# Kernel optimization log

Hardware: AMD Instinct MI355X
Metric: run time of the kernel (lower is better)

The kernel has to match this reference:

```python
import jax, jax.numpy as jnp
import numpy as np

B, K, D = 16384, 64, 128


def setup_inputs() -> dict:
    key = jax.random.key(0)
    kx, kc = jax.random.split(key)
    x = jax.random.normal(kx, (B, D), dtype=jnp.float32)
    centers = jax.random.uniform(kc, (K, D), dtype=jnp.float32)  # torch.rand init
    return {"x": x, "centers": centers}


def reference(x, centers):
    batch, dim = x.shape
    k = centers.shape[0]
    # pairwise squared distances, same math as sum((x - c)^2)
    diff = x[:, None, :] - centers[None, :, :]          # [B, K, D]
    dist_sq = jnp.sum(diff * diff, axis=-1)             # [B, K]
    expo = -0.5 * dist_sq
    # safe softmax over clusters (identical to max-subtracted exp/sum)
    resp = jax.nn.softmax(expo, axis=-1)                # [B, K]
    log_resp = jnp.log(jnp.clip(resp, 1e-8))
    # hard assignment and per-cluster statistics
    assign = jnp.argmin(dist_sq, axis=-1)               # [B] int
    onehot = jax.nn.one_hot(assign, k, dtype=x.dtype)   # [B, K]
    cluster_weight = jnp.sum(onehot, axis=0)            # [K]
    emp_total = jnp.einsum('nk,nd->kd', onehot, x)      # [K, D]
    emp_mean = emp_total / (cluster_weight[:, None] + 1e-7)
    # masked centered samples: onehot[n,k]*(x_n - mean_k) is nonzero only at k=assign(n)
    xm = x - emp_mean[assign]                           # [B, D]
    covar_total = jnp.einsum('nk,nd,ne->kde', onehot, xm, xm)  # [K, D, D]
    covar = covar_total / (cluster_weight[:, None, None] + 1e-7)
    eye = jnp.eye(dim, dtype=x.dtype)
    covar_diag = covar * eye
    covar_off = covar * (1.0 - eye)
    diag_dist_sq = jnp.sum((covar_diag - eye) ** 2, axis=(1, 2))  # [K]
    off_dist_sq = jnp.sum(covar_off ** 2, axis=(1, 2))            # [K]
    mean_dist_sq = jnp.sum((emp_mean - centers) ** 2, axis=1)     # [K]
    mean_mse = jnp.sum(cluster_weight * mean_dist_sq) / (batch * dim)
    covar_mse = jnp.sum(
        cluster_weight * diag_dist_sq / (batch * dim)
        + cluster_weight * off_dist_sq / (batch * dim * (dim - 1.0))
    )
    return log_resp, mean_mse, covar_mse
```

## Files before the change

kernel.cpp:

```cpp
#include <hip/hip_runtime.h>

#define BB 16384
#define KK 64
#define DD 128
#define SEG 256
#define MAXITEMS 128
#define NRB 4
#define RSLAB 4096
#define RBLKS (KK * NRB)

typedef __attribute__((ext_vector_type(8))) short bf16x8;
typedef __attribute__((ext_vector_type(4))) float f32x4;

__device__ __forceinline__ unsigned int packbf2(float a, float b) {
    unsigned ua = __float_as_uint(a);
    unsigned ub = __float_as_uint(b);
    ua = (ua + 0x7FFFu + ((ua >> 16) & 1u)) >> 16;
    ub = (ub + 0x7FFFu + ((ub >> 16) & 1u)) >> 16;
    return ua | (ub << 16);
}

__global__ __launch_bounds__(256) void k_rows(
    const float* __restrict__ x, const float* __restrict__ centers,
    float* __restrict__ log_resp, int* __restrict__ assign,
    int* __restrict__ bhist, int* __restrict__ counter)
{
    __shared__ float xs[64][132];
    __shared__ float ct[DD][66];
    __shared__ float cn2[KK];
    __shared__ int   lh[KK];

    const int tid = threadIdx.x;
    const int row0 = blockIdx.x * 64;

    if (blockIdx.x == 0 && tid == 0) *counter = 0;
    if (tid < KK) lh[tid] = 0;

    for (int g = tid; g < 64 * 32; g += 256) {
        int r = g >> 5, c4 = g & 31;
        float4 v = ((const float4*)(x + (size_t)(row0 + r) * DD))[c4];
        *(float4*)&xs[r][c4 * 4] = v;
    }
    for (int g = tid; g < KK * 32; g += 256) {
        int k = g >> 5, c4 = g & 31;
        float4 v = ((const float4*)(centers + (size_t)k * DD))[c4];
        ct[c4 * 4 + 0][k] = v.x;
        ct[c4 * 4 + 1][k] = v.y;
        ct[c4 * 4 + 2][k] = v.z;
        ct[c4 * 4 + 3][k] = v.w;
    }
    __syncthreads();
    if (tid < KK) {
        float s = 0.f;
        for (int d = 0; d < DD; ++d) { float c = ct[d][tid]; s = fmaf(c, c, s); }
        cn2[tid] = s;
    }
    __syncthreads();

    const int tr = tid >> 5;
    const int tc = tid & 31;
    const int k0 = tc * 2, k1 = k0 + 1;

    float acc0[8], acc1[8];
    #pragma unroll
    for (int i = 0; i < 8; ++i) { acc0[i] = 0.f; acc1[i] = 0.f; }

    for (int d = 0; d < DD; d += 4) {
        float2 b0 = *(const float2*)&ct[d + 0][k0];
        float2 b1 = *(const float2*)&ct[d + 1][k0];
        float2 b2 = *(const float2*)&ct[d + 2][k0];
        float2 b3 = *(const float2*)&ct[d + 3][k0];
        #pragma unroll
        for (int i = 0; i < 8; ++i) {
            float4 a = *(const float4*)&xs[tr * 8 + i][d];
            acc0[i] = fmaf(a.x, b0.x, acc0[i]);
            acc1[i] = fmaf(a.x, b0.y, acc1[i]);
            acc0[i] = fmaf(a.y, b1.x, acc0[i]);
            acc1[i] = fmaf(a.y, b1.y, acc1[i]);
            acc0[i] = fmaf(a.z, b2.x, acc0[i]);
            acc1[i] = fmaf(a.z, b2.y, acc1[i]);
            acc0[i] = fmaf(a.w, b3.x, acc0[i]);
            acc1[i] = fmaf(a.w, b3.y, acc1[i]);
        }
    }

    const float cn0 = 0.5f * cn2[k0], cn1 = 0.5f * cn2[k1];
    #pragma unroll
    for (int i = 0; i < 8; ++i) {
        int row = row0 + tr * 8 + i;
        float v0 = acc0[i] - cn0;
        float v1 = acc1[i] - cn1;
        float m; int idx;
        if (v1 > v0) { m = v1; idx = k1; } else { m = v0; idx = k0; }
        #pragma unroll
        for (int off = 1; off < 32; off <<= 1) {
            float ov = __shfl_xor(m, off);
            int   oi = __shfl_xor(idx, off);
            if (ov > m || (ov == m && oi < idx)) { m = ov; idx = oi; }
        }
        float s = expf(v0 - m) + expf(v1 - m);
        #pragma unroll
        for (int off = 1; off < 32; off <<= 1) s += __shfl_xor(s, off);
        float ls = logf(s);
        float lr0 = fmaxf(v0 - m - ls, -18.4206807f);
        float lr1 = fmaxf(v1 - m - ls, -18.4206807f);
        *(float2*)&log_resp[(size_t)row * KK + k0] = make_float2(lr0, lr1);
        if (tc == 0) {
            assign[row] = idx;
            atomicAdd(&lh[idx], 1);
        }
    }
    __syncthreads();
    if (tid < KK) bhist[blockIdx.x * KK + tid] = lh[tid];
}

__global__ __launch_bounds__(256) void k_scat(
    const int* __restrict__ assign, const int* __restrict__ bhist,
    int* __restrict__ sorted, float* __restrict__ cw,
    int4* __restrict__ items, int* __restrict__ item_count,
    int* __restrict__ ist, int* __restrict__ ien)
{
    __shared__ int ph_tot[4][KK], ph_pre[4][KK];
    __shared__ int cnt_s[KK], pre_s[KK], base_s[KK], cur_s[KK];

    const int tid = threadIdx.x;
    const int b = blockIdx.x;
    const int t = tid & 63, q = tid >> 6;

    int tot = 0, pre = 0;
    const int bb0 = q * 64;
    for (int bb = bb0; bb < bb0 + 64; ++bb) {
        int v = bhist[bb * KK + t];
        tot += v;
        if (bb < b) pre += v;
    }
    ph_tot[q][t] = tot; ph_pre[q][t] = pre;
    __syncthreads();

    if (tid < KK) {
        cnt_s[tid] = ph_tot[0][tid] + ph_tot[1][tid] + ph_tot[2][tid] + ph_tot[3][tid];
        pre_s[tid] = ph_pre[0][tid] + ph_pre[1][tid] + ph_pre[2][tid] + ph_pre[3][tid];
        cur_s[tid] = 0;
    }
    __syncthreads();
    if (tid == 0) {
        int base = 0;
        for (int k = 0; k < KK; ++k) { base_s[k] = base; base += cnt_s[k]; }
    }
    __syncthreads();

    if (tid < 64) {
        int r = b * 64 + tid;
        int a = assign[r];
        int p = base_s[a] + pre_s[a] + atomicAdd(&cur_s[a], 1);
        sorted[p] = r;
    }

    if (b == 0) {
        if (tid < KK) cw[tid] = (float)cnt_s[tid];
        if (tid == 0) {
            int ic = 0;
            for (int k = 0; k < KK; ++k) {
                ist[k] = ic;
                int c = cnt_s[k];
                for (int s = 0; s < c; s += SEG) {
                    int4 it; it.x = k; it.y = base_s[k] + s;
                    it.z = min(SEG, c - s); it.w = 0;
                    items[ic++] = it;
                }
                ien[k] = ic;
            }
            *item_count = ic;
        }
    }
}

__global__ __launch_bounds__(256) void k_seg(
    const float* __restrict__ x, const int* __restrict__ sorted,
    const int4* __restrict__ items, const int* __restrict__ item_count,
    float* __restrict__ part, float* __restrict__ emp_part)
{
    if ((int)blockIdx.x >= *item_count) return;
    int4 it = items[blockIdx.x];
    const int gstart = it.y, len = it.z;

    __shared__ int rows_s[128];
    __shared__ unsigned int XT[DD][68];

    const int tid = threadIdx.x;
    const int w = tid >> 6, lane = tid & 63;
    const int c4 = lane & 15, q = lane >> 4;

    f32x4 acc[2][8];
    #pragma unroll
    for (int h = 0; h < 2; ++h)
        #pragma unroll
        for (int nt = 0; nt < 8; ++nt)
            acc[h][nt] = (f32x4){0.f, 0.f, 0.f, 0.f};
    float colsum = 0.f;

    for (int half = 0; half < 2; ++half) {
        const int hoff = half * 128;
        const int hlen = min(128, len - hoff);
        if (hlen <= 0) break;

        __syncthreads();
        if (tid < hlen) rows_s[tid] = sorted[gstart + hoff + tid];
        __syncthreads();

        {
            const int r0 = 2 * lane, r1 = 2 * lane + 1;
            const int d0 = w * 32;
            const float* p0 = x + (size_t)rows_s[r0 < hlen ? r0 : 0] * DD + d0;
            const float* p1 = x + (size_t)rows_s[r1 < hlen ? r1 : 0] * DD + d0;
            #pragma unroll
            for (int i = 0; i < 8; ++i) {
                float4 a = make_float4(0.f, 0.f, 0.f, 0.f);
                float4 b = make_float4(0.f, 0.f, 0.f, 0.f);
                if (r0 < hlen) a = *(const float4*)(p0 + 4 * i);
                if (r1 < hlen) b = *(const float4*)(p1 + 4 * i);
                XT[d0 + 4 * i + 0][lane] = packbf2(a.x, b.x);
                XT[d0 + 4 * i + 1][lane] = packbf2(a.y, b.y);
                XT[d0 + 4 * i + 2][lane] = packbf2(a.z, b.z);
                XT[d0 + 4 * i + 3][lane] = packbf2(a.w, b.w);
            }
        }
        __syncthreads();

        if (tid < DD) {
            float s = 0.f;
            #pragma unroll
            for (int j4 = 0; j4 < 16; ++j4) {
                uint4 v = *(const uint4*)&XT[tid][j4 * 4];
                s += __uint_as_float(v.x << 16) + __uint_as_float(v.x & 0xFFFF0000u);
                s += __uint_as_float(v.y << 16) + __uint_as_float(v.y & 0xFFFF0000u);
                s += __uint_as_float(v.z << 16) + __uint_as_float(v.z & 0xFFFF0000u);
                s += __uint_as_float(v.w << 16) + __uint_as_float(v.w & 0xFFFF0000u);
            }
            colsum += s;
        }

        #pragma unroll
        for (int c = 0; c < 4; ++c) {
            const int ku = c * 16 + q * 4;
            bf16x8 a0 = *(const bf16x8*)&XT[(2 * w + 0) * 16 + c4][ku];
            bf16x8 a1 = *(const bf16x8*)&XT[(2 * w + 1) * 16 + c4][ku];
            #pragma unroll
            for (int nt = 0; nt < 8; ++nt) {
                bf16x8 b = *(const bf16x8*)&XT[nt * 16 + c4][ku];
                acc[0][nt] = __builtin_amdgcn_mfma_f32_16x16x32_bf16(a0, b, acc[0][nt], 0, 0, 0);
                acc[1][nt] = __builtin_amdgcn_mfma_f32_16x16x32_bf16(a1, b, acc[1][nt], 0, 0, 0);
            }
        }
    }

    if (tid < DD) emp_part[blockIdx.x * DD + tid] = colsum;

    float* pb = part + (size_t)blockIdx.x * (DD * DD);
    #pragma unroll
    for (int h = 0; h < 2; ++h) {
        const int m0 = (2 * w + h) * 16 + q * 4;
        #pragma unroll
        for (int nt = 0; nt < 8; ++nt) {
            const int n = nt * 16 + c4;
            pb[(m0 + 0) * DD + n] = acc[h][nt].x;
            pb[(m0 + 1) * DD + n] = acc[h][nt].y;
            pb[(m0 + 2) * DD + n] = acc[h][nt].z;
            pb[(m0 + 3) * DD + n] = acc[h][nt].w;
        }
    }
}

__global__ __launch_bounds__(256) void k_redfinal(
    const float* __restrict__ part, const float* __restrict__ emp_part,
    const float* __restrict__ cw, const float* __restrict__ centers,
    const int* __restrict__ ist, const int* __restrict__ ien,
    float2* __restrict__ spart, int* __restrict__ counter,
    float* __restrict__ outscalars)
{
    const int k = blockIdx.x >> 2;
    const int p = blockIdx.x & 3;
    const int i0 = ist[k], i1 = ien[k];
    const int tid = threadIdx.x;
    const int w = tid >> 6, lane = tid & 63;
    const float wgt = cw[k];
    const float inv = 1.0f / (wgt + 1e-7f);

    __shared__ float mu_s[DD], emp_s[DD];
    __shared__ float emp2[2][DD];
    __shared__ float red[4][RSLAB];

    {
        const int dh = tid & 127, hf = tid >> 7;
        float e0 = 0.f, e1 = 0.f;
        int it = i0 + hf;
        for (; it + 2 < i1; it += 4) {
            e0 += emp_part[it * DD + dh];
            e1 += emp_part[(it + 2) * DD + dh];
        }
        if (it < i1) e0 += emp_part[it * DD + dh];
        emp2[hf][dh] = e0 + e1;
    }
    __syncthreads();
    if (tid < DD) {
        float e = emp2[0][tid] + emp2[1][tid];
        emp_s[tid] = e;
        mu_s[tid] = e * inv;
    }

    float4 acc[16];
    #pragma unroll
    for (int c = 0; c < 16; ++c) acc[c] = make_float4(0.f, 0.f, 0.f, 0.f);

    const int base = p * RSLAB;
    for (int it = i0 + w; it < i1; it += 4) {
        const float* pb = part + (size_t)it * (DD * DD) + base;
        #pragma unroll
        for (int c = 0; c < 16; ++c) {
            float4 v = *(const float4*)&pb[c * 256 + lane * 4];
            acc[c].x += v.x; acc[c].y += v.y; acc[c].z += v.z; acc[c].w += v.w;
        }
    }
    #pragma unroll
    for (int c = 0; c < 16; ++c)
        *(float4*)&red[w][c * 256 + lane * 4] = acc[c];
    __syncthreads();

    float ds = 0.f, os = 0.f, mm = 0.f;
    #pragma unroll
    for (int jj = 0; jj < 16; ++jj) {
        int el = jj * 256 + tid;
        float sx = red[0][el] + red[1][el] + red[2][el] + red[3][el];
        int gel = base + el;
        int d = gel >> 7, e = gel & 127;
        float ctv = sx - mu_s[d] * emp_s[e] - emp_s[d] * mu_s[e]
                  + wgt * mu_s[d] * mu_s[e];
        float v = ctv * inv;
        if (d == e) { float t = v - 1.f; ds += t * t; }
        else        { os += v * v; }
    }
    if (p == 0 && tid < DD) {
        float t = mu_s[tid] - centers[k * DD + tid];
        mm = t * t;
    }

    #pragma unroll
    for (int off = 32; off > 0; off >>= 1) {
        ds += __shfl_down(ds, off);
        os += __shfl_down(os, off);
        mm += __shfl_down(mm, off);
    }
    __shared__ float rds[4], ros[4], rmm[4];
    __shared__ int is_last;
    if (lane == 0) { rds[w] = ds; ros[w] = os; rmm[w] = mm; }
    __syncthreads();
    if (tid == 0) {
        float DS = rds[0] + rds[1] + rds[2] + rds[3];
        float OS = ros[0] + ros[1] + ros[2] + ros[3];
        float MM = rmm[0] + rmm[1] + rmm[2] + rmm[3];
        const float bd = (float)BB * (float)DD;
        float2 mine;
        mine.x = wgt * MM / bd;
        mine.y = wgt * DS / bd + wgt * OS / (bd * (float)(DD - 1));
        spart[blockIdx.x] = mine;
        __threadfence();
        int old = atomicAdd(counter, 1);
        is_last = (old == RBLKS - 1);
    }
    __syncthreads();
    if (is_last) {
        __threadfence();
        float2 v = (tid < RBLKS) ? spart[tid] : make_float2(0.f, 0.f);
        float a = v.x, b = v.y;
        #pragma unroll
        for (int off = 32; off > 0; off >>= 1) {
            a += __shfl_down(a, off);
            b += __shfl_down(b, off);
        }
        __shared__ float ra[4], rb[4];
        if (lane == 0) { ra[w] = a; rb[w] = b; }
        __syncthreads();
        if (tid == 0) {
            outscalars[0] = ra[0] + ra[1] + ra[2] + ra[3];
            outscalars[1] = rb[0] + rb[1] + rb[2] + rb[3];
        }
    }
}

extern "C" void kernel_launch(void* const* d_in, const int* in_sizes, int n_in,
                              void* d_out, int out_size, void* d_ws, size_t ws_size,
                              hipStream_t stream) {
    const float* x = (const float*)d_in[0];
    const float* centers = (const float*)d_in[1];
    float* out = (float*)d_out;
    float* outscalars = out + (size_t)BB * KK;

    char* ws = (char*)d_ws;
    size_t off = 0;
    float*  part     = (float*)(ws + off); off += (size_t)MAXITEMS * DD * DD * 4;
    float*  emp_part = (float*)(ws + off); off += MAXITEMS * DD * 4;
    int*    sorted   = (int*)  (ws + off); off += BB * 4;
    int*    assign   = (int*)  (ws + off); off += BB * 4;
    int*    bhist    = (int*)  (ws + off); off += 256 * KK * 4;
    int4*   items    = (int4*) (ws + off); off += 256 * 16;
    float*  cw       = (float*)(ws + off); off += 256;
    int*    itemcnt  = (int*)  (ws + off); off += 256;
    int*    ist      = (int*)  (ws + off); off += 256;
    int*    ien      = (int*)  (ws + off); off += 256;
    float2* spart    = (float2*)(ws + off); off += RBLKS * 8;
    int*    counter  = (int*)  (ws + off); off += 256;

    k_rows    <<<256, 256, 0, stream>>>(x, centers, out, assign, bhist, counter);
    k_scat    <<<256, 256, 0, stream>>>(assign, bhist, sorted, cw, items,
                                        itemcnt, ist, ien);
    k_seg     <<<MAXITEMS, 256, 0, stream>>>(x, sorted, items, itemcnt,
                                             part, emp_part);
    k_redfinal<<<RBLKS, 256, 0, stream>>>(part, emp_part, cw, centers, ist, ien,
                                          spart, counter, outscalars);
}
```

Measured before the change: 126.5 us.

## Fuse scatter, segment GEMM and reduction into one kernel with grid barrier

Merges the three post-assignment kernels into one persistent 256-block kernel. Each block recomputes the cluster histogram and segment table itself and gathers its segment's row indices by ballot-scanning the assign array, so the global sorted array is no longer needed. A software grid barrier on an atomic counter then separates the covariance-GEMM phase from the reduction phase. This removes two launches and the sorted/items round trips. In exchange every block scans up to all of assign, and the spin barrier assumes all 256 blocks are co-resident.

```diff
diff --git a/kernel.cpp b/kernel.cpp
--- a/kernel.cpp
+++ b/kernel.cpp
@@ -7,7 +7,7 @@
 #define MAXITEMS 128
 #define NRB 4
 #define RSLAB 4096
-#define RBLKS (KK * NRB)
+#define NBLK 256
 
 typedef __attribute__((ext_vector_type(8))) short bf16x8;
 typedef __attribute__((ext_vector_type(4))) float f32x4;
@@ -23,7 +23,7 @@
 __global__ __launch_bounds__(256) void k_rows(
     const float* __restrict__ x, const float* __restrict__ centers,
     float* __restrict__ log_resp, int* __restrict__ assign,
-    int* __restrict__ bhist, int* __restrict__ counter)
+    int* __restrict__ bhist, int* __restrict__ counters)
 {
     __shared__ float xs[64][132];
     __shared__ float ct[DD][66];
@@ -33,7 +33,7 @@
     const int tid = threadIdx.x;
     const int row0 = blockIdx.x * 64;
 
-    if (blockIdx.x == 0 && tid == 0) *counter = 0;
+    if (blockIdx.x == 0 && tid < 2) counters[tid] = 0;
     if (tid < KK) lh[tid] = 0;
 
     for (int g = tid; g < 64 * 32; g += 256) {
@@ -114,275 +114,276 @@
     if (tid < KK) bhist[blockIdx.x * KK + tid] = lh[tid];
 }
 
-__global__ __launch_bounds__(256) void k_scat(
-    const int* __restrict__ assign, const int* __restrict__ bhist,
-    int* __restrict__ sorted, float* __restrict__ cw,
-    int4* __restrict__ items, int* __restrict__ item_count,
-    int* __restrict__ ist, int* __restrict__ ien)
+__global__ __launch_bounds__(256) void k_main(
+    const float* __restrict__ x, const int* __restrict__ assign,
+    const int* __restrict__ bhist, const float* __restrict__ centers,
+    float* __restrict__ part, float* __restrict__ emp_part,
+    float2* __restrict__ spart, int* __restrict__ counters,
+    float* __restrict__ outscalars)
 {
-    __shared__ int ph_tot[4][KK], ph_pre[4][KK];
-    __shared__ int cnt_s[KK], pre_s[KK], base_s[KK], cur_s[KK];
+    __shared__ __align__(16) char smem[65536];
+    unsigned int (*XT)[68] = (unsigned int (*)[68])smem;
+    int* rows_s = (int*)(smem + 34816);
+    float (*red)[RSLAB] = (float (*)[RSLAB])smem;
+
+    __shared__ int ph_tot[4][KK];
+    __shared__ int cnt_s[KK], ist_s[KK], ien_s[KK];
+    __shared__ int wtot[4];
+    __shared__ int myk_s, myseg_s;
 
     const int tid = threadIdx.x;
     const int b = blockIdx.x;
-    const int t = tid & 63, q = tid >> 6;
-
-    int tot = 0, pre = 0;
-    const int bb0 = q * 64;
-    for (int bb = bb0; bb < bb0 + 64; ++bb) {
-        int v = bhist[bb * KK + t];
-        tot += v;
-        if (bb < b) pre += v;
-    }
-    ph_tot[q][t] = tot; ph_pre[q][t] = pre;
-    __syncthreads();
-
-    if (tid < KK) {
+    const int w = tid >> 6, lane = tid & 63;
+    int* bar1 = counters;
+    int* fincnt = counters + 1;
+
+    {
+        const int t = tid & 63, q = tid >> 6;
+        int tot = 0;
+        for (int bb = q * 64; bb < q * 64 + 64; ++bb)
+            tot += bhist[bb * KK + t];
+        ph_tot[q][t] = tot;
+    }
+    __syncthreads();
+    if (tid < KK)
         cnt_s[tid] = ph_tot[0][tid] + ph_tot[1][tid] + ph_tot[2][tid] + ph_tot[3][tid];
-        pre_s[tid] = ph_pre[0][tid] + ph_pre[1][tid] + ph_pre[2][tid] + ph_pre[3][tid];
-        cur_s[tid] = 0;
-    }
     __syncthreads();
     if (tid == 0) {
-        int base = 0;
-        for (int k = 0; k < KK; ++k) { base_s[k] = base; base += cnt_s[k]; }
-    }
-    __syncthreads();
-
-    if (tid < 64) {
-        int r = b * 64 + tid;
-        int a = assign[r];
-        int p = base_s[a] + pre_s[a] + atomicAdd(&cur_s[a], 1);
-        sorted[p] = r;
-    }
-
-    if (b == 0) {
-        if (tid < KK) cw[tid] = (float)cnt_s[tid];
-        if (tid == 0) {
-            int ic = 0;
-            for (int k = 0; k < KK; ++k) {
-                ist[k] = ic;
-                int c = cnt_s[k];
-                for (int s = 0; s < c; s += SEG) {
-                    int4 it; it.x = k; it.y = base_s[k] + s;
-                    it.z = min(SEG, c - s); it.w = 0;
-                    items[ic++] = it;
+        int ic = 0;
+        myk_s = -1;
+        for (int k = 0; k < KK; ++k) {
+            ist_s[k] = ic;
+            int ns = (cnt_s[k] + SEG - 1) / SEG;
+            if (b >= ic && b < ic + ns) { myk_s = k; myseg_s = b - ic; }
+            ic += ns;
+            ien_s[k] = ic;
+        }
+    }
+    __syncthreads();
+
+    if (myk_s >= 0) {
+        const int kC = myk_s;
+        const int lo = myseg_s * SEG;
+        const int hi = min(lo + SEG, cnt_s[kC]);
+        const int len = hi - lo;
+
+        {
+            int running = 0;
+            for (int c = 0; c < BB / 256; ++c) {
+                if (running >= hi) break;
+                int a = assign[c * 256 + tid];
+                bool m = (a == kC);
+                unsigned long long bal = __ballot(m);
+                if (lane == 0) wtot[w] = __popcll(bal);
+                __syncthreads();
+                int woff = 0;
+                #pragma unroll
+                for (int j = 0; j < 4; ++j) if (j < w) woff += wtot[j];
+                int ctot = wtot[0] + wtot[1] + wtot[2] + wtot[3];
+                if (m) {
+                    int rank = __popcll(bal & ((1ull << lane) - 1ull));
+                    int pos = running + woff + rank;
+                    if (pos >= lo && pos < hi) rows_s[pos - lo] = c * 256 + tid;
                 }
-                ien[k] = ic;
-            }
-            *item_count = ic;
-        }
-    }
-}
-
-__global__ __launch_bounds__(256) void k_seg(
-    const float* __restrict__ x, const int* __restrict__ sorted,
-    const int4* __restrict__ items, const int* __restrict__ item_count,
-    float* __restrict__ part, float* __restrict__ emp_part)
-{
-    if ((int)blockIdx.x >= *item_count) return;
-    int4 it = items[blockIdx.x];
-    const int gstart = it.y, len = it.z;
-
-    __shared__ int rows_s[128];
-    __shared__ unsigned int XT[DD][68];
-
-    const int tid = threadIdx.x;
-    const int w = tid >> 6, lane = tid & 63;
-    const int c4 = lane & 15, q = lane >> 4;
-
-    f32x4 acc[2][8];
-    #pragma unroll
-    for (int h = 0; h < 2; ++h)
-        #pragma unroll
-        for (int nt = 0; nt < 8; ++nt)
-            acc[h][nt] = (f32x4){0.f, 0.f, 0.f, 0.f};
-    float colsum = 0.f;
-
-    for (int half = 0; half < 2; ++half) {
-        const int hoff = half * 128;
-        const int hlen = min(128, len - hoff);
-        if (hlen <= 0) break;
-
-        __syncthreads();
-        if (tid < hlen) rows_s[tid] = sorted[gstart + hoff + tid];
-        __syncthreads();
-
-        {
-            const int r0 = 2 * lane, r1 = 2 * lane + 1;
-            const int d0 = w * 32;
-            const float* p0 = x + (size_t)rows_s[r0 < hlen ? r0 : 0] * DD + d0;
-            const float* p1 = x + (size_t)rows_s[r1 < hlen ? r1 : 0] * DD + d0;
+                running += ctot;
+                __syncthreads();
+            }
+        }
+
+        const int c4 = lane & 15, q = lane >> 4;
+        f32x4 acc[2][8];
+        #pragma unroll
+        for (int h = 0; h < 2; ++h)
             #pragma unroll
-            for (int i = 0; i < 8; ++i) {
-                float4 a = make_float4(0.f, 0.f, 0.f, 0.f);
-                float4 b = make_float4(0.f, 0.f, 0.f, 0.f);
-                if (r0 < hlen) a = *(const float4*)(p0 + 4 * i);
-                if (r1 < hlen) b = *(const float4*)(p1 + 4 * i);
-                XT[d0 + 4 * i + 0][lane] = packbf2(a.x, b.x);
-                XT[d0 + 4 * i + 1][lane] = packbf2(a.y, b.y);
-                XT[d0 + 4 * i + 2][lane] = packbf2(a.z, b.z);
-                XT[d0 + 4 * i + 3][lane] = packbf2(a.w, b.w);
-            }
-        }
-        __syncthreads();
-
-        if (tid < DD) {
-            float s = 0.f;
+            for (int nt = 0; nt < 8; ++nt)
+                acc[h][nt] = (f32x4){0.f, 0.f, 0.f, 0.f};
+        float colsum = 0.f;
+
+        for (int half = 0; half < 2; ++half) {
+            const int hoff = half * 128;
+            const int hlen = min(128, len - hoff);
+            if (hlen <= 0) break;
+
+            __syncthreads();
+            {
+                const int r0 = 2 * lane, r1 = 2 * lane + 1;
+                const int d0 = w * 32;
+                const float* p0 = x + (size_t)rows_s[hoff + (r0 < hlen ? r0 : 0)] * DD + d0;
+                const float* p1 = x + (size_t)rows_s[hoff + (r1 < hlen ? r1 : 0)] * DD + d0;
+                #pragma unroll
+                for (int i = 0; i < 8; ++i) {
+                    float4 a = make_float4(0.f, 0.f, 0.f, 0.f);
+                    float4 bb = make_float4(0.f, 0.f, 0.f, 0.f);
+                    if (r0 < hlen) a  = *(const float4*)(p0 + 4 * i);
+                    if (r1 < hlen) bb = *(const float4*)(p1 + 4 * i);
+                    XT[d0 + 4 * i + 0][lane] = packbf2(a.x, bb.x);
+                    XT[d0 + 4 * i + 1][lane] = packbf2(a.y, bb.y);
+                    XT[d0 + 4 * i + 2][lane] = packbf2(a.z, bb.z);
+                    XT[d0 + 4 * i + 3][lane] = packbf2(a.w, bb.w);
+                }
+            }
+            __syncthreads();
+
+            if (tid < DD) {
+                float s = 0.f;
+                #pragma unroll
+                for (int j4 = 0; j4 < 16; ++j4) {
+                    uint4 v = *(const uint4*)&XT[tid][j4 * 4];
+                    s += __uint_as_float(v.x << 16) + __uint_as_float(v.x & 0xFFFF0000u);
+                    s += __uint_as_float(v.y << 16) + __uint_as_float(v.y & 0xFFFF0000u);
+                    s += __uint_as_float(v.z << 16) + __uint_as_float(v.z & 0xFFFF0000u);
+                    s += __uint_as_float(v.w << 16) + __uint_as_float(v.w & 0xFFFF0000u);
+                }
+                colsum += s;
+            }
+
             #pragma unroll
-            for (int j4 = 0; j4 < 16; ++j4) {
-                uint4 v = *(const uint4*)&XT[tid][j4 * 4];
-                s += __uint_as_float(v.x << 16) + __uint_as_float(v.x & 0xFFFF0000u);
-                s += __uint_as_float(v.y << 16) + __uint_as_float(v.y & 0xFFFF0000u);
-                s += __uint_as_float(v.z << 16) + __uint_as_float(v.z & 0xFFFF0000u);
-                s += __uint_as_float(v.w << 16) + __uint_as_float(v.w & 0xFFFF0000u);
-            }
-            colsum += s;
-        }
-
-        #pragma unroll
-        for (int c = 0; c < 4; ++c) {
-            const int ku = c * 16 + q * 4;
-            bf16x8 a0 = *(const bf16x8*)&XT[(2 * w + 0) * 16 + c4][ku];
-            bf16x8 a1 = *(const bf16x8*)&XT[(2 * w + 1) * 16 + c4][ku];
+            for (int c = 0; c < 4; ++c) {
+                const int ku = c * 16 + q * 4;
+                bf16x8 a0 = *(const bf16x8*)&XT[(2 * w + 0) * 16 + c4][ku];
+                bf16x8 a1 = *(const bf16x8*)&XT[(2 * w + 1) * 16 + c4][ku];
+                #pragma unroll
+                for (int nt = 0; nt < 8; ++nt) {
+                    bf16x8 bb = *(const bf16x8*)&XT[nt * 16 + c4][ku];
+                    acc[0][nt] = __builtin_amdgcn_mfma_f32_16x16x32_bf16(a0, bb, acc[0][nt], 0, 0, 0);
+                    acc[1][nt] = __builtin_amdgcn_mfma_f32_16x16x32_bf16(a1, bb, acc[1][nt], 0, 0, 0);
+                }
+            }
+        }
+
+        if (tid < DD) emp_part[b * DD + tid] = colsum;
+
+        float* pb = part + (size_t)b * (DD * DD);
+        #pragma unroll
+        for (int h = 0; h < 2; ++h) {
+            const int m0 = (2 * w + h) * 16 + q * 4;
             #pragma unroll
             for (int nt = 0; nt < 8; ++nt) {
-                bf16x8 b = *(const bf16x8*)&XT[nt * 16 + c4][ku];
-                acc[0][nt] = __builtin_amdgcn_mfma_f32_16x16x32_bf16(a0, b, acc[0][nt], 0, 0, 0);
-                acc[1][nt] = __builtin_amdgcn_mfma_f32_16x16x32_bf16(a1, b, acc[1][nt], 0, 0, 0);
-            }
-        }
-    }
-
-    if (tid < DD) emp_part[blockIdx.x * DD + tid] = colsum;
-
-    float* pb = part + (size_t)blockIdx.x * (DD * DD);
-    #pragma unroll
-    for (int h = 0; h < 2; ++h) {
-        const int m0 = (2 * w + h) * 16 + q * 4;
-        #pragma unroll
-        for (int nt = 0; nt < 8; ++nt) {
-            const int n = nt * 16 + c4;
-            pb[(m0 + 0) * DD + n] = acc[h][nt].x;
-            pb[(m0 + 1) * DD + n] = acc[h][nt].y;
-            pb[(m0 + 2) * DD + n] = acc[h][nt].z;
-            pb[(m0 + 3) * DD + n] = acc[h][nt].w;
-        }
-    }
-}
-
-__global__ __launch_bounds__(256) void k_redfinal(
-    const float* __restrict__ part, const float* __restrict__ emp_part,
-    const float* __restrict__ cw, const float* __restrict__ centers,
-    const int* __restrict__ ist, const int* __restrict__ ien,
-    float2* __restrict__ spart, int* __restrict__ counter,
-    float* __restrict__ outscalars)
-{
-    const int k = blockIdx.x >> 2;
-    const int p = blockIdx.x & 3;
-    const int i0 = ist[k], i1 = ien[k];
-    const int tid = threadIdx.x;
-    const int w = tid >> 6, lane = tid & 63;
-    const float wgt = cw[k];
-    const float inv = 1.0f / (wgt + 1e-7f);
-
-    __shared__ float mu_s[DD], emp_s[DD];
-    __shared__ float emp2[2][DD];
-    __shared__ float red[4][RSLAB];
+                const int n = nt * 16 + c4;
+                pb[(m0 + 0) * DD + n] = acc[h][nt].x;
+                pb[(m0 + 1) * DD + n] = acc[h][nt].y;
+                pb[(m0 + 2) * DD + n] = acc[h][nt].z;
+                pb[(m0 + 3) * DD + n] = acc[h][nt].w;
+            }
+        }
+    }
+
+    __syncthreads();
+    if (tid == 0) {
+        __threadfence();
+        atomicAdd(bar1, 1);
+        while (__hip_atomic_load(bar1, __ATOMIC_ACQUIRE,
+                                 __HIP_MEMORY_SCOPE_AGENT) < NBLK)
+            __builtin_amdgcn_s_sleep(8);
+    }
+    __syncthreads();
+    __threadfence();
 
     {
-        const int dh = tid & 127, hf = tid >> 7;
-        float e0 = 0.f, e1 = 0.f;
-        int it = i0 + hf;
-        for (; it + 2 < i1; it += 4) {
-            e0 += emp_part[it * DD + dh];
-            e1 += emp_part[(it + 2) * DD + dh];
-        }
-        if (it < i1) e0 += emp_part[it * DD + dh];
-        emp2[hf][dh] = e0 + e1;
-    }
-    __syncthreads();
-    if (tid < DD) {
-        float e = emp2[0][tid] + emp2[1][tid];
-        emp_s[tid] = e;
-        mu_s[tid] = e * inv;
-    }
-
-    float4 acc[16];
-    #pragma unroll
-    for (int c = 0; c < 16; ++c) acc[c] = make_float4(0.f, 0.f, 0.f, 0.f);
-
-    const int base = p * RSLAB;
-    for (int it = i0 + w; it < i1; it += 4) {
-        const float* pb = part + (size_t)it * (DD * DD) + base;
-        #pragma unroll
-        for (int c = 0; c < 16; ++c) {
-            float4 v = *(const float4*)&pb[c * 256 + lane * 4];
-            acc[c].x += v.x; acc[c].y += v.y; acc[c].z += v.z; acc[c].w += v.w;
-        }
-    }
-    #pragma unroll
-    for (int c = 0; c < 16; ++c)
-        *(float4*)&red[w][c * 256 + lane * 4] = acc[c];
-    __syncthreads();
-
-    float ds = 0.f, os = 0.f, mm = 0.f;
-    #pragma unroll
-    for (int jj = 0; jj < 16; ++jj) {
-        int el = jj * 256 + tid;
-        float sx = red[0][el] + red[1][el] + red[2][el] + red[3][el];
-        int gel = base + el;
-        int d = gel >> 7, e = gel & 127;
-        float ctv = sx - mu_s[d] * emp_s[e] - emp_s[d] * mu_s[e]
-                  + wgt * mu_s[d] * mu_s[e];
-        float v = ctv * inv;
-        if (d == e) { float t = v - 1.f; ds += t * t; }
-        else        { os += v * v; }
-    }
-    if (p == 0 && tid < DD) {
-        float t = mu_s[tid] - centers[k * DD + tid];
-        mm = t * t;
-    }
-
-    #pragma unroll
-    for (int off = 32; off > 0; off >>= 1) {
-        ds += __shfl_down(ds, off);
-        os += __shfl_down(os, off);
-        mm += __shfl_down(mm, off);
-    }
-    __shared__ float rds[4], ros[4], rmm[4];
-    __shared__ int is_last;
-    if (lane == 0) { rds[w] = ds; ros[w] = os; rmm[w] = mm; }
-    __syncthreads();
-    if (tid == 0) {
-        float DS = rds[0] + rds[1] + rds[2] + rds[3];
-        float OS = ros[0] + ros[1] + ros[2] + ros[3];
-        float MM = rmm[0] + rmm[1] + rmm[2] + rmm[3];
-        const float bd = (float)BB * (float)DD;
-        float2 mine;
-        mine.x = wgt * MM / bd;
-        mine.y = wgt * DS / bd + wgt * OS / (bd * (float)(DD - 1));
-        spart[blockIdx.x] = mine;
-        __threadfence();
-        int old = atomicAdd(counter, 1);
-        is_last = (old == RBLKS - 1);
-    }
-    __syncthreads();
-    if (is_last) {
-        __threadfence();
-        float2 v = (tid < RBLKS) ? spart[tid] : make_float2(0.f, 0.f);
-        float a = v.x, b = v.y;
+        const int kD = b >> 2;
+        const int p = b & 3;
+        const int i0 = ist_s[kD], i1 = ien_s[kD];
+        const float wgt = (float)cnt_s[kD];
+        const float inv = 1.0f / (wgt + 1e-7f);
+
+        __shared__ float mu_s[DD], emp_s[DD];
+        __shared__ float emp2[2][DD];
+
+        {
+            const int dh = tid & 127, hf = tid >> 7;
+            float e0 = 0.f, e1 = 0.f;
+            int it = i0 + hf;
+            for (; it + 2 < i1; it += 4) {
+                e0 += emp_part[it * DD + dh];
+                e1 += emp_part[(it + 2) * DD + dh];
+            }
+            if (it < i1) e0 += emp_part[it * DD + dh];
+            emp2[hf][dh] = e0 + e1;
+        }
+        __syncthreads();
+        if (tid < DD) {
+            float e = emp2[0][tid] + emp2[1][tid];
+            emp_s[tid] = e;
+            mu_s[tid] = e * inv;
+        }
+
+        float4 acc[16];
+        #pragma unroll
+        for (int c = 0; c < 16; ++c) acc[c] = make_float4(0.f, 0.f, 0.f, 0.f);
+
+        const int base = p * RSLAB;
+        for (int it = i0 + w; it < i1; it += 4) {
+            const float* pb = part + (size_t)it * (DD * DD) + base;
+            #pragma unroll
+            for (int c = 0; c < 16; ++c) {
+                float4 v = *(const float4*)&pb[c * 256 + lane * 4];
+                acc[c].x += v.x; acc[c].y += v.y; acc[c].z += v.z; acc[c].w += v.w;
+            }
+        }
+        __syncthreads();
+        #pragma unroll
+        for (int c = 0; c < 16; ++c)
+            *(float4*)&red[w][c * 256 + lane * 4] = acc[c];
+        __syncthreads();
+
+        float ds = 0.f, os = 0.f, mm = 0.f;
+        #pragma unroll
+        for (int jj = 0; jj < 16; ++jj) {
+            int el = jj * 256 + tid;
+            float sx = red[0][el] + red[1][el] + red[2][el] + red[3][el];
+            int gel = base + el;
+            int d = gel >> 7, e = gel & 127;
+            float ctv = sx - mu_s[d] * emp_s[e] - emp_s[d] * mu_s[e]
+                      + wgt * mu_s[d] * mu_s[e];
+            float v = ctv * inv;
+            if (d == e) { float t = v - 1.f; ds += t * t; }
+            else        { os += v * v; }
+        }
+        if (p == 0 && tid < DD) {
+            float t = mu_s[tid] - centers[kD * DD + tid];
+            mm = t * t;
+        }
+
         #pragma unroll
         for (int off = 32; off > 0; off >>= 1) {
-            a += __shfl_down(a, off);
-            b += __shfl_down(b, off);
-        }
-        __shared__ float ra[4], rb[4];
-        if (lane == 0) { ra[w] = a; rb[w] = b; }
+            ds += __shfl_down(ds, off);
+            os += __shfl_down(os, off);
+            mm += __shfl_down(mm, off);
+        }
+        __shared__ float rds[4], ros[4], rmm[4];
+        __shared__ int is_last;
+        if (lane == 0) { rds[w] = ds; ros[w] = os; rmm[w] = mm; }
         __syncthreads();
         if (tid == 0) {
-            outscalars[0] = ra[0] + ra[1] + ra[2] + ra[3];
-            outscalars[1] = rb[0] + rb[1] + rb[2] + rb[3];
+            float DS = rds[0] + rds[1] + rds[2] + rds[3];
+            float OS = ros[0] + ros[1] + ros[2] + ros[3];
+            float MM = rmm[0] + rmm[1] + rmm[2] + rmm[3];
+            const float bd = (float)BB * (float)DD;
+            float2 mine;
+            mine.x = wgt * MM / bd;
+            mine.y = wgt * DS / bd + wgt * OS / (bd * (float)(DD - 1));
+            spart[b] = mine;
+            __threadfence();
+            int old = atomicAdd(fincnt, 1);
+            is_last = (old == NBLK - 1);
+        }
+        __syncthreads();
+        if (is_last) {
+            __threadfence();
+            float2 v = (tid < NBLK) ? spart[tid] : make_float2(0.f, 0.f);
+            float a = v.x, bb = v.y;
+            #pragma unroll
+            for (int off = 32; off > 0; off >>= 1) {
+                a  += __shfl_down(a, off);
+                bb += __shfl_down(bb, off);
+            }
+            __shared__ float ra[4], rb[4];
+            if (lane == 0) { ra[w] = a; rb[w] = bb; }
+            __syncthreads();
+            if (tid == 0) {
+                outscalars[0] = ra[0] + ra[1] + ra[2] + ra[3];
+                outscalars[1] = rb[0] + rb[1] + rb[2] + rb[3];
+            }
         }
     }
 }
@@ -399,22 +400,12 @@
     size_t off = 0;
     float*  part     = (float*)(ws + off); off += (size_t)MAXITEMS * DD * DD * 4;
     float*  emp_part = (float*)(ws + off); off += MAXITEMS * DD * 4;
-    int*    sorted   = (int*)  (ws + off); off += BB * 4;
     int*    assign   = (int*)  (ws + off); off += BB * 4;
     int*    bhist    = (int*)  (ws + off); off += 256 * KK * 4;
-    int4*   items    = (int4*) (ws + off); off += 256 * 16;
-    float*  cw       = (float*)(ws + off); off += 256;
-    int*    itemcnt  = (int*)  (ws + off); off += 256;
-    int*    ist      = (int*)  (ws + off); off += 256;
-    int*    ien      = (int*)  (ws + off); off += 256;
-    float2* spart    = (float2*)(ws + off); off += RBLKS * 8;
-    int*    counter  = (int*)  (ws + off); off += 256;
-
-    k_rows    <<<256, 256, 0, stream>>>(x, centers, out, assign, bhist, counter);
-    k_scat    <<<256, 256, 0, stream>>>(assign, bhist, sorted, cw, items,
-                                        itemcnt, ist, ien);
-    k_seg     <<<MAXITEMS, 256, 0, stream>>>(x, sorted, items, itemcnt,
-                                             part, emp_part);
-    k_redfinal<<<RBLKS, 256, 0, stream>>>(part, emp_part, cw, centers, ist, ien,
-                                          spart, counter, outscalars);
+    float2* spart    = (float2*)(ws + off); off += NBLK * 8;
+    int*    counters = (int*)  (ws + off); off += 256;
+
+    k_rows<<<256, 256, 0, stream>>>(x, centers, out, assign, bhist, counters);
+    k_main<<<NBLK, 256, 0, stream>>>(x, assign, bhist, centers, part, emp_part,
+                                     spart, counters, outscalars);
 }
```

Result: slower. 274.5 us (+117.1%).
